# Kernel tuning notes

Hardware: AMD Instinct MI355X
Metric: run time of the kernel (lower is better)

The kernel has to match this reference:

```python
import jax, jax.numpy as jnp
import numpy as np

B, T, S = 16, 128, 128          # batch, temporal, spatial (road segments)
NIN, SIN = 3, 1                 # number / speed input feature sizes
NH, SH, DH = 64, 64, 128        # number-enc / speed-enc / decoder hidden
T_PREDICT = 20


def _p(k, shape, scale=0.05):
    return (jax.random.normal(k, shape) * scale).astype(jnp.float32)


def setup_inputs() -> dict:
    key = jax.random.key(0)
    ks = jax.random.split(key, 16)
    inp = {"input_data": jax.random.normal(ks[0], (B, T, S, NIN + SIN), dtype=jnp.float32)}
    # seg_model cells: LSTM gates driven by input x, own hidden h, spatial neighbors h_after/h_before
    inp.update(
        n_Wx=_p(ks[1], (NIN, 4 * NH)), n_Wh=_p(ks[2], (NH, 4 * NH)),
        n_Wa=_p(ks[3], (NH, 4 * NH)), n_Wb=_p(ks[4], (NH, 4 * NH)),
        n_b=jnp.zeros((4 * NH,), jnp.float32),
        s_Wx=_p(ks[5], (SIN, 4 * SH)), s_Wh=_p(ks[6], (SH, 4 * SH)),
        s_Wa=_p(ks[7], (SH, 4 * SH)), s_Wb=_p(ks[8], (SH, 4 * SH)),
        s_b=jnp.zeros((4 * SH,), jnp.float32),
        d_Wx=_p(ks[9], (NH + SH, 4 * DH)), d_Wh=_p(ks[10], (DH, 4 * DH)),
        d_Wa=_p(ks[11], (DH, 4 * DH)), d_Wb=_p(ks[12], (DH, 4 * DH)),
        d_b=jnp.zeros((4 * DH,), jnp.float32),
        on_W=_p(ks[13], (DH, 1)), on_b=jnp.zeros((1,), jnp.float32),
        os_W=_p(ks[14], (DH, 1)), os_b=jnp.zeros((1,), jnp.float32),
    )
    return inp


def _cell(x, h, c, ha, hb, Wx, Wh, Wa, Wb, b):
    g = x @ Wx + h @ Wh + ha @ Wa + hb @ Wb + b
    i, f, u, o = jnp.split(g, 4, axis=-1)
    c2 = jax.nn.sigmoid(f) * c + jax.nn.sigmoid(i) * jnp.tanh(u)
    return jax.nn.sigmoid(o) * jnp.tanh(c2), c2


def _shift(h):
    # h_after[s] = h[s+1], h_before[s] = h[s-1], zero-padded at the boundary
    z = jnp.zeros_like(h[:, :1])
    return jnp.concatenate([h[:, 1:], z], axis=1), jnp.concatenate([z, h[:, :-1]], axis=1)


def _next_input(former_number, next_x, output):
    # output: [B,S,2] = (number_out, speed_out)
    speed_in = next_x[:, :1, 3:]                                    # [B,1,1]
    speed_next = jnp.concatenate([speed_in, output[:, 1:, 1:]], axis=1)
    inflow = jnp.concatenate([next_x[:, 0:1, 1:2], output[:, :-1, 0:1]], axis=1)
    number_calc = former_number[:, :, 2:3] + inflow - output[:, :, 0:1]
    return jnp.concatenate([output[:, :, 0:1], inflow, number_calc, speed_next], axis=2)


def reference(input_data, n_Wx, n_Wh, n_Wa, n_Wb, n_b,
              s_Wx, s_Wh, s_Wa, s_Wb, s_b,
              d_Wx, d_Wh, d_Wa, d_Wb, d_b,
              on_W, on_b, os_W, os_b):
    b, t, s, _ = input_data.shape
    zeros = lambda hdim: jnp.zeros((b, s, hdim), input_data.dtype)
    init = (zeros(NH), zeros(NH), zeros(SH), zeros(SH), zeros(DH), zeros(DH))

    def step(carry, xs):
        hn, cn, hs, cs, hd, cd = carry
        x_t, x_tp1 = xs
        hn_a, hn_b = _shift(hn)
        hs_a, hs_b = _shift(hs)
        hd_a, hd_b = _shift(hd)
        num = x_t[:, :, :NIN]
        spd = x_t[:, :, NIN:]
        hn, cn = _cell(num, hn, cn, hn_a, hn_b, n_Wx, n_Wh, n_Wa, n_Wb, n_b)
        hs, cs = _cell(spd, hs, cs, hs_a, hs_b, s_Wx, s_Wh, s_Wa, s_Wb, s_b)
        dec_in = jnp.concatenate([hn, hs], axis=2)
        hd, cd = _cell(dec_in, hd, cd, hd_a, hd_b, d_Wx, d_Wh, d_Wa, d_Wb, d_b)
        output = jnp.concatenate([hd @ on_W + on_b, hd @ os_W + os_b], axis=2)
        data = _next_input(num, x_tp1, output)
        return (hn, cn, hs, cs, hd, cd), data

    xs = (jnp.moveaxis(input_data[:, :-1], 1, 0),   # x_t,   t = 0..T-2 (time-major)
          jnp.moveaxis(input_data[:, 1:], 1, 0))    # x_{t+1}
    _, datas = jax.lax.scan(step, init, xs)          # [T-1, B, S, 4]
    # original writes outputs only for time >= t_predict; slicing is equivalent
    return jnp.moveaxis(datas[T_PREDICT:], 0, 1)     # [B, T-T_PREDICT-1, S, 4]
```

## Files before the change

### kernel.cpp

```cpp
#include <hip/hip_runtime.h>

constexpr int B_ = 16, T_ = 128, S_ = 128;
constexpr int ROWS = B_ * S_;
constexpr int NSTEPS = T_ - 1;
constexpr int TPRED = 20;
constexpr int TOUT = NSTEPS - TPRED;
constexpr int TB = 512;
constexpr int NBLK = 160;

constexpr int OFF_HN = 0;
constexpr int OFF_HS = OFF_HN + 262144;
constexpr int OFF_HD = OFF_HS + 262144;
constexpr int OFF_BAR = OFF_HD + 262144;
constexpr int OFF_OUTS = OFF_BAR + 8192;
constexpr int OFF_NPK = OFF_OUTS + NSTEPS * ROWS * 2;
constexpr int NPK_DW = 16 * 7 * 256;
constexpr int OFF_SPK = OFF_NPK + NPK_DW;
constexpr int OFF_DPK = OFF_SPK + NPK_DW;
constexpr int DPK_DW = 32 * 16 * 256;
constexpr int PACK_DWORDS = 2 * NPK_DW + DPK_DW;
constexpr int ZERO_DW = OFF_NPK;

typedef _Float16 half8 __attribute__((ext_vector_type(8)));
typedef float float4v __attribute__((ext_vector_type(4)));
typedef unsigned long long ull;

__device__ __forceinline__ float sigm(float x) { return 1.f / (1.f + __expf(-x)); }
__device__ __forceinline__ float tanh_(float x) { return 2.f / (1.f + __expf(-2.f * x)) - 1.f; }
__device__ __forceinline__ unsigned int pack2(float a, float b) {
    union { unsigned int u; _Float16 h[2]; } x;
    x.h[0] = (_Float16)a; x.h[1] = (_Float16)b; return x.u;
}

__device__ __forceinline__ unsigned ld_dev_u32(const unsigned* p) {
    return __hip_atomic_load(p, __ATOMIC_RELAXED, __HIP_MEMORY_SCOPE_AGENT);
}
__device__ __forceinline__ ull ld_dev_u64(const ull* p) {
    return __hip_atomic_load(p, __ATOMIC_RELAXED, __HIP_MEMORY_SCOPE_AGENT);
}
__device__ __forceinline__ void st_dev_u64(ull* p, ull v) {
    __hip_atomic_store(p, v, __ATOMIC_RELAXED, __HIP_MEMORY_SCOPE_AGENT);
}
__device__ __forceinline__ void st_dev_f16(_Float16* p, _Float16 v) {
    __hip_atomic_store(p, v, __ATOMIC_RELAXED, __HIP_MEMORY_SCOPE_AGENT);
}
__device__ __forceinline__ void at_add_u32(unsigned* p, unsigned v) {
    __hip_atomic_fetch_add(p, v, __ATOMIC_RELAXED, __HIP_MEMORY_SCOPE_AGENT);
}
__device__ __forceinline__ void at_add_f32(float* p, float v) {
    __hip_atomic_fetch_add(p, v, __ATOMIC_RELAXED, __HIP_MEMORY_SCOPE_AGENT);
}

__global__ __launch_bounds__(256) void pack_weights(
    const float* __restrict__ nWx, const float* __restrict__ nWh,
    const float* __restrict__ nWa, const float* __restrict__ nWb, const float* __restrict__ nb,
    const float* __restrict__ sWx, const float* __restrict__ sWh,
    const float* __restrict__ sWa, const float* __restrict__ sWb, const float* __restrict__ sb,
    const float* __restrict__ dWx, const float* __restrict__ dWh,
    const float* __restrict__ dWa, const float* __restrict__ dWb,
    unsigned int* __restrict__ wsu)
{
    int idx = blockIdx.x * 256 + threadIdx.x;
    if (idx >= PACK_DWORDS) return;
    if (idx < 2 * NPK_DW) {
        bool isS = idx >= NPK_DW;
        int dn = isS ? idx - NPK_DW : idx;
        int tile = dn >> 8;
        int e = (dn & 255) * 2;
        int lane = e >> 3, j0 = e & 7;
        int quad = lane >> 4;
        int nt = tile / 7, tt = tile % 7;
        int col = nt * 16 + (lane & 15);
        float v0, v1;
        if (tt < 6) {
            const float* W = isS ? ((tt < 2) ? sWh : (tt < 4) ? sWa : sWb)
                                 : ((tt < 2) ? nWh : (tt < 4) ? nWa : nWb);
            int k = (tt & 1) * 32 + quad * 8 + j0;
            v0 = W[k * 256 + col]; v1 = W[(k + 1) * 256 + col];
        } else {
            int kl = quad * 8 + j0;
            auto xv = [&](int k) -> float {
                if (!isS) { if (k < 3) return nWx[k * 256 + col]; if (k == 3) return nb[col]; return 0.f; }
                else      { if (k == 4) return sWx[col]; if (k == 5) return sb[col]; return 0.f; }
            };
            v0 = xv(kl); v1 = xv(kl + 1);
        }
        wsu[(isS ? OFF_SPK : OFF_NPK) + dn] = pack2(v0, v1);
    } else {
        int dd = idx - 2 * NPK_DW;
        int tile = dd >> 8;
        int e = (dd & 255) * 2;
        int lane = e >> 3, j0 = e & 7;
        int quad = lane >> 4;
        int nt = tile >> 4, tt = tile & 15;
        const float* W = (tt < 4) ? dWx : (tt < 8) ? dWh : (tt < 12) ? dWa : dWb;
        int k = (tt & 3) * 32 + quad * 8 + j0;
        int col = nt * 16 + (lane & 15);
        wsu[OFF_DPK + dd] = pack2(W[k * 512 + col], W[(k + 1) * 512 + col]);
    }
}

__global__ __launch_bounds__(TB) void pipe_persist(
    const float* __restrict__ input,
    const float* __restrict__ db,
    const float* __restrict__ onW, const float* __restrict__ onb,
    const float* __restrict__ osW, const float* __restrict__ osb,
    float* __restrict__ ws)
{
    const int tid = threadIdx.x;
    const int wave = tid >> 6, lane = tid & 63;
    const int quad = lane >> 4, l15 = lane & 15;
    const int blk = blockIdx.x;

    unsigned* wsu = (unsigned*)ws;
    unsigned* hnU = wsu + OFF_HN;
    unsigned* hsU = wsu + OFF_HS;
    unsigned* hdU = wsu + OFF_HD;
    unsigned* nsc = wsu + OFF_BAR;
    unsigned* dc  = wsu + OFF_BAR + 1024;
    float* outs = ws + OFF_OUTS;

    union SMem {
        struct {
            _Float16 pk[16 * 7 * 512];
            _Float16 hst[2][130][72];
            _Float16 xa[128][40];
        } ns;
        struct {
            _Float16 wd[4 * 16 * 512];
            _Float16 dec[128][136];
            _Float16 hd[130][136];
            _Float16 hpub[128][16];
        } d;
    };
    __shared__ __align__(16) SMem sm;

    if (blk < 32) {
        const bool isS = (blk >= 16);
        const int rg = blk & 15;
        _Float16* hH = (_Float16*)(isS ? hsU : hnU);
        unsigned* dcp = dc + rg * 32;

        const ull* pkG = (const ull*)(wsu + (isS ? OFF_SPK : OFF_NPK));
        for (int i = tid; i < 14336; i += TB) ((ull*)sm.ns.pk)[i] = pkG[i];
        for (int i = tid; i < 9360; i += TB) ((unsigned*)sm.ns.hst)[i] = 0u;
        for (int i = tid; i < 2560; i += TB) ((unsigned*)sm.ns.xa)[i] = 0u;
        float4v c4[4];
#pragma unroll
        for (int cg = 0; cg < 4; ++cg) c4[cg] = (float4v){0.f, 0.f, 0.f, 0.f};
        __syncthreads();

        for (int e = 0; e < NSTEPS; ++e) {
            const int pinL = (e + 1) & 1, poutL = e & 1;
            const int poutG = e & 3;
            if (tid < 128) {
                const float* xp = input + ((size_t)(rg * T_ + e) * S_ + tid) * 4;
                unsigned* row = (unsigned*)sm.ns.xa + tid * 20;
                row[0] = pack2(xp[0], xp[1]);
                row[1] = pack2(xp[2], 1.f);
                row[2] = pack2(xp[3], 1.f);
            }
            if (e >= 4) {
                unsigned tgt = 8u * (unsigned)(e - 3);
                while (ld_dev_u32(dcp) < tgt) __builtin_amdgcn_s_sleep(1);
            }
            __syncthreads();

            const _Float16* hb = &sm.ns.hst[pinL][0][0];
            const int ri = wave * 16 + l15;
            half8 ah0 = *(const half8*)(hb + (ri + 1) * 72 + quad * 8);
            half8 ah1 = *(const half8*)(hb + (ri + 1) * 72 + 32 + quad * 8);
            half8 aa0 = *(const half8*)(hb + (ri + 2) * 72 + quad * 8);
            half8 aa1 = *(const half8*)(hb + (ri + 2) * 72 + 32 + quad * 8);
            half8 ab0 = *(const half8*)(hb + (ri) * 72 + quad * 8);
            half8 ab1 = *(const half8*)(hb + (ri) * 72 + 32 + quad * 8);
            half8 ax  = *(const half8*)(&sm.ns.xa[0][0] + ri * 40 + quad * 8);
            _Float16* hLp = &sm.ns.hst[poutL][0][0];
            _Float16* hGp = hH + (size_t)poutG * 131072 + (size_t)rg * 128 * 64;
#pragma unroll
            for (int cg = 0; cg < 4; ++cg) {
                float4v acc[4];
#pragma unroll
                for (int g = 0; g < 4; ++g) acc[g] = (float4v){0.f, 0.f, 0.f, 0.f};
#pragma unroll
                for (int g = 0; g < 4; ++g) {
                    const _Float16* base = sm.ns.pk + (size_t)(4 * g + cg) * 7 * 512 + lane * 8;
                    acc[g] = __builtin_amdgcn_mfma_f32_16x16x32_f16(ah0, *(const half8*)(base),        acc[g], 0, 0, 0);
                    acc[g] = __builtin_amdgcn_mfma_f32_16x16x32_f16(ah1, *(const half8*)(base + 512),  acc[g], 0, 0, 0);
                    acc[g] = __builtin_amdgcn_mfma_f32_16x16x32_f16(aa0, *(const half8*)(base + 1024), acc[g], 0, 0, 0);
                    acc[g] = __builtin_amdgcn_mfma_f32_16x16x32_f16(aa1, *(const half8*)(base + 1536), acc[g], 0, 0, 0);
                    acc[g] = __builtin_amdgcn_mfma_f32_16x16x32_f16(ab0, *(const half8*)(base + 2048), acc[g], 0, 0, 0);
                    acc[g] = __builtin_amdgcn_mfma_f32_16x16x32_f16(ab1, *(const half8*)(base + 2560), acc[g], 0, 0, 0);
                    acc[g] = __builtin_amdgcn_mfma_f32_16x16x32_f16(ax,  *(const half8*)(base + 3072), acc[g], 0, 0, 0);
                }
                const int kcol = cg * 16 + l15;
                float4v cold = c4[cg], cnew;
#pragma unroll
                for (int r = 0; r < 4; ++r) {
                    float c2 = sigm(acc[1][r]) * cold[r] + sigm(acc[0][r]) * tanh_(acc[2][r]);
                    float h2 = sigm(acc[3][r]) * tanh_(c2);
                    cnew[r] = c2;
                    int row = wave * 16 + quad * 4 + r;
                    _Float16 hf = (_Float16)h2;
                    hLp[(row + 1) * 72 + kcol] = hf;
                    st_dev_f16(hGp + (size_t)row * 64 + kcol, hf);
                }
                c4[cg] = cnew;
            }
            asm volatile("s_waitcnt vmcnt(0)" ::: "memory");
            __syncthreads();
            if (tid == 0) at_add_u32(nsc + rg * 32, 1u);
        }
    } else {
        const int idx = blk - 32;
        const int rg = idx >> 3;
        const int c = idx & 7;
        const int r0 = rg * 128;
        unsigned* dcp = dc + rg * 32;
        unsigned* nscp = nsc + rg * 32;

        const ull* pdG = (const ull*)(wsu + OFF_DPK);
        for (int i = tid; i < 8192; i += TB) {
            int tile = i >> 7, j = i & 127;
            int g = tile >> 4, tt = tile & 15;
            ((ull*)sm.d.wd)[(g * 16 + tt) * 128 + j] =
                pdG[(size_t)((g * 8 + c) * 16 + tt) * 128 + j];
        }
        if (tid < 68) {
            ((unsigned*)&sm.d.hd[0][0])[tid] = 0u;
            ((unsigned*)&sm.d.hd[129][0])[tid] = 0u;
        }
        const int hcol = c * 16 + l15;
        const float won = onW[hcol], wos = osW[hcol];
        float bg[4];
#pragma unroll
        for (int g = 0; g < 4; ++g) bg[g] = db[g * 128 + hcol];
        float4v creg = (float4v){0.f, 0.f, 0.f, 0.f};
        __syncthreads();

        for (int e = 1; e <= NSTEPS; ++e) {
            const int t = e - 1;
            const int pdec = t & 3;
            const int phdin = e & 1;
            const int phdout = t & 1;
            if (e >= 2) {
                unsigned tgt = 8u * (unsigned)(e - 1);
                while (ld_dev_u32(dcp) < tgt) __builtin_amdgcn_s_sleep(1);
            }
            {
                unsigned tgt = 2u * (unsigned)e;
                while (ld_dev_u32(nscp) < tgt) __builtin_amdgcn_s_sleep(1);
            }
            const ull* srcH = (const ull*)(hdU + (size_t)phdin * 131072);
#pragma unroll
            for (int i = tid; i < 4096; i += TB) {
                int row = i >> 5, j = i & 31;
                *((ull*)&sm.d.hd[row + 1][0] + j) = ld_dev_u64(srcH + (size_t)(r0 + row) * 32 + j);
            }
            const ull* srcN = (const ull*)(hnU + (size_t)pdec * 32768);
            const ull* srcS = (const ull*)(hsU + (size_t)pdec * 32768);
#pragma unroll
            for (int i = tid; i < 4096; i += TB) {
                int hf = i >> 11, j2 = i & 2047;
                int row = j2 >> 4, j = j2 & 15;
                *((ull*)&sm.d.dec[row][hf * 64] + j) =
                    ld_dev_u64((hf ? srcS : srcN) + (size_t)(r0 + row) * 16 + j);
            }
            __syncthreads();

            const int ri = wave * 16 + l15;
            half8 fr[16];
#pragma unroll
            for (int kt = 0; kt < 4; ++kt) {
                fr[kt]      = *(const half8*)(&sm.d.dec[ri][0] + kt * 32 + quad * 8);
                fr[4 + kt]  = *(const half8*)(&sm.d.hd[ri + 1][0] + kt * 32 + quad * 8);
                fr[8 + kt]  = *(const half8*)(&sm.d.hd[ri + 2][0] + kt * 32 + quad * 8);
                fr[12 + kt] = *(const half8*)(&sm.d.hd[ri][0] + kt * 32 + quad * 8);
            }
            float4v acc[4];
#pragma unroll
            for (int g = 0; g < 4; ++g) acc[g] = (float4v){0.f, 0.f, 0.f, 0.f};
#pragma unroll
            for (int g = 0; g < 4; ++g) {
                const _Float16* bw = sm.d.wd + (size_t)(g * 16) * 512 + lane * 8;
#pragma unroll
                for (int kt = 0; kt < 16; ++kt)
                    acc[g] = __builtin_amdgcn_mfma_f32_16x16x32_f16(fr[kt], *(const half8*)(bw + kt * 512), acc[g], 0, 0, 0);
            }
            float4v cold = creg, cnew;
#pragma unroll
            for (int r = 0; r < 4; ++r) {
                float c2 = sigm(acc[1][r] + bg[1]) * cold[r] + sigm(acc[0][r] + bg[0]) * tanh_(acc[2][r] + bg[2]);
                float h2 = sigm(acc[3][r] + bg[3]) * tanh_(c2);
                cnew[r] = c2;
                int row = wave * 16 + quad * 4 + r;
                sm.d.hpub[row][l15] = (_Float16)h2;
                float pon = h2 * won, pos = h2 * wos;
#pragma unroll
                for (int off = 8; off; off >>= 1) {
                    pon += __shfl_down(pon, off, 16);
                    pos += __shfl_down(pos, off, 16);
                }
                if (l15 == 0) {
                    float* o = outs + ((size_t)t * ROWS + (r0 + row)) * 2;
                    at_add_f32(o, pon);
                    at_add_f32(o + 1, pos);
                }
            }
            creg = cnew;
            __syncthreads();
            {
                int prow = tid >> 2, jj = tid & 3;
                ull v = *((const ull*)&sm.d.hpub[prow][0] + jj);
                st_dev_u64((ull*)hdU + (size_t)phdout * 65536 + (size_t)(r0 + prow) * 32 + c * 4 + jj, v);
            }
            asm volatile("s_waitcnt vmcnt(0)" ::: "memory");
            __syncthreads();
            if (tid == 0) at_add_u32(dcp, 1u);
        }
    }
}

__global__ __launch_bounds__(256) void assemble_kernel(
    const float* __restrict__ input, const float* __restrict__ ws, float* __restrict__ out,
    const float* __restrict__ onb, const float* __restrict__ osb)
{
    const float* outs = ws + OFF_OUTS;
    int idx = blockIdx.x * 256 + threadIdx.x;
    if (idx >= B_ * TOUT * S_) return;
    float b_on = onb[0], b_os = osb[0];
    int s = idx & 127;
    int tmp = idx >> 7;
    int tt = tmp % TOUT;
    int b = tmp / TOUT;
    int t = tt + TPRED;
    int row = b * S_ + s;
    float o0 = outs[((size_t)t * ROWS + row) * 2 + 0] + b_on;
    float o1 = outs[((size_t)t * ROWS + row) * 2 + 1] + b_os;
    float inflow = (s == 0) ? input[(((size_t)b * T_ + (t + 1)) * S_ + 0) * 4 + 1]
                            : (outs[((size_t)t * ROWS + row - 1) * 2 + 0] + b_on);
    float numc = input[(((size_t)b * T_ + t) * S_ + s) * 4 + 2] + inflow - o0;
    float spd = (s == 0) ? input[(((size_t)b * T_ + (t + 1)) * S_ + 0) * 4 + 3] : o1;
    float4 v = make_float4(o0, inflow, numc, spd);
    reinterpret_cast<float4*>(out)[idx] = v;
}

extern "C" void kernel_launch(void* const* d_in, const int* in_sizes, int n_in,
                              void* d_out, int out_size, void* d_ws, size_t ws_size,
                              hipStream_t stream) {
    const float* input = (const float*)d_in[0];
    const float* nWx = (const float*)d_in[1];
    const float* nWh = (const float*)d_in[2];
    const float* nWa = (const float*)d_in[3];
    const float* nWb = (const float*)d_in[4];
    const float* nb  = (const float*)d_in[5];
    const float* sWx = (const float*)d_in[6];
    const float* sWh = (const float*)d_in[7];
    const float* sWa = (const float*)d_in[8];
    const float* sWb = (const float*)d_in[9];
    const float* sb  = (const float*)d_in[10];
    const float* dWx = (const float*)d_in[11];
    const float* dWh = (const float*)d_in[12];
    const float* dWa = (const float*)d_in[13];
    const float* dWb = (const float*)d_in[14];
    const float* db  = (const float*)d_in[15];
    const float* onW = (const float*)d_in[16];
    const float* onb = (const float*)d_in[17];
    const float* osW = (const float*)d_in[18];
    const float* osb = (const float*)d_in[19];

    float* ws = (float*)d_ws;

    hipMemsetAsync(ws, 0, (size_t)ZERO_DW * 4, stream);

    pack_weights<<<dim3((PACK_DWORDS + 255) / 256), dim3(256), 0, stream>>>(
        nWx, nWh, nWa, nWb, nb, sWx, sWh, sWa, sWb, sb,
        dWx, dWh, dWa, dWb, (unsigned int*)ws);

    void* kargs[] = {
        (void*)&input, (void*)&db, (void*)&onW, (void*)&onb,
        (void*)&osW, (void*)&osb, (void*)&ws
    };
    hipLaunchCooperativeKernel((void*)pipe_persist, dim3(NBLK), dim3(TB),
                               kargs, 0, stream);

    int nout = B_ * TOUT * S_;
    assemble_kernel<<<dim3((nout + 255) / 256), dim3(256), 0, stream>>>(
        input, ws, (float*)d_out, onb, osb);
}
```

Baseline: 1.317 ms.

## Batch hidden-state publishes and reorder decoder waits to overlap loads with signaling

Encoder blocks now write their hidden state to shared memory only, then publish it to global memory with coalesced 64-bit stores after a barrier, replacing scattered per-element f16 atomic stores. Decoder blocks wait on the encoder counter first and load the encoder outputs before waiting on the decoder-neighbor counter, with loads batched into registers. The decoder also signals its step completion before the output-projection atomics, which shortens the critical path between dependent blocks. This adds an extra barrier in the encoder and keeps more registers live for the staged loads.

```diff
diff --git a/kernel.cpp b/kernel.cpp
--- a/kernel.cpp
+++ b/kernel.cpp
@@ -41,15 +41,13 @@
 __device__ __forceinline__ void st_dev_u64(ull* p, ull v) {
     __hip_atomic_store(p, v, __ATOMIC_RELAXED, __HIP_MEMORY_SCOPE_AGENT);
 }
-__device__ __forceinline__ void st_dev_f16(_Float16* p, _Float16 v) {
-    __hip_atomic_store(p, v, __ATOMIC_RELAXED, __HIP_MEMORY_SCOPE_AGENT);
-}
 __device__ __forceinline__ void at_add_u32(unsigned* p, unsigned v) {
     __hip_atomic_fetch_add(p, v, __ATOMIC_RELAXED, __HIP_MEMORY_SCOPE_AGENT);
 }
 __device__ __forceinline__ void at_add_f32(float* p, float v) {
     __hip_atomic_fetch_add(p, v, __ATOMIC_RELAXED, __HIP_MEMORY_SCOPE_AGENT);
 }
+#define WAIT_VM0() asm volatile("s_waitcnt vmcnt(0)" ::: "memory")
 
 __global__ __launch_bounds__(256) void pack_weights(
     const float* __restrict__ nWx, const float* __restrict__ nWh,
@@ -113,9 +111,9 @@
     const int blk = blockIdx.x;
 
     unsigned* wsu = (unsigned*)ws;
-    unsigned* hnU = wsu + OFF_HN;
-    unsigned* hsU = wsu + OFF_HS;
-    unsigned* hdU = wsu + OFF_HD;
+    char* hnB = (char*)(wsu + OFF_HN);
+    char* hsB = (char*)(wsu + OFF_HS);
+    char* hdB = (char*)(wsu + OFF_HD);
     unsigned* nsc = wsu + OFF_BAR;
     unsigned* dc  = wsu + OFF_BAR + 1024;
     float* outs = ws + OFF_OUTS;
@@ -138,8 +136,9 @@
     if (blk < 32) {
         const bool isS = (blk >= 16);
         const int rg = blk & 15;
-        _Float16* hH = (_Float16*)(isS ? hsU : hnU);
+        char* hB = isS ? hsB : hnB;
         unsigned* dcp = dc + rg * 32;
+        unsigned* nscp = nsc + rg * 32;
 
         const ull* pkG = (const ull*)(wsu + (isS ? OFF_SPK : OFF_NPK));
         for (int i = tid; i < 14336; i += TB) ((ull*)sm.ns.pk)[i] = pkG[i];
@@ -176,7 +175,6 @@
             half8 ab1 = *(const half8*)(hb + (ri) * 72 + 32 + quad * 8);
             half8 ax  = *(const half8*)(&sm.ns.xa[0][0] + ri * 40 + quad * 8);
             _Float16* hLp = &sm.ns.hst[poutL][0][0];
-            _Float16* hGp = hH + (size_t)poutG * 131072 + (size_t)rg * 128 * 64;
 #pragma unroll
             for (int cg = 0; cg < 4; ++cg) {
                 float4v acc[4];
@@ -201,15 +199,24 @@
                     float h2 = sigm(acc[3][r]) * tanh_(c2);
                     cnew[r] = c2;
                     int row = wave * 16 + quad * 4 + r;
-                    _Float16 hf = (_Float16)h2;
-                    hLp[(row + 1) * 72 + kcol] = hf;
-                    st_dev_f16(hGp + (size_t)row * 64 + kcol, hf);
+                    hLp[(row + 1) * 72 + kcol] = (_Float16)h2;
                 }
                 c4[cg] = cnew;
             }
-            asm volatile("s_waitcnt vmcnt(0)" ::: "memory");
-            __syncthreads();
-            if (tid == 0) at_add_u32(nsc + rg * 32, 1u);
+            __syncthreads();
+            {
+                char* dst0 = hB + (size_t)poutG * 262144 + (size_t)rg * 16384;
+#pragma unroll
+                for (int k = 0; k < 4; ++k) {
+                    int i = tid + k * 512;
+                    int row = i >> 4, j = i & 15;
+                    ull v = *((const ull*)&sm.ns.hst[poutL][row + 1][0] + j);
+                    st_dev_u64((ull*)(dst0 + (size_t)row * 128 + (size_t)j * 8), v);
+                }
+            }
+            WAIT_VM0();
+            __syncthreads();
+            if (tid == 0) at_add_u32(nscp, 1u);
         }
     } else {
         const int idx = blk - 32;
@@ -243,28 +250,46 @@
             const int pdec = t & 3;
             const int phdin = e & 1;
             const int phdout = t & 1;
+            {
+                unsigned tgt = 2u * (unsigned)e;
+                while (ld_dev_u32(nscp) < tgt) __builtin_amdgcn_s_sleep(1);
+            }
+            {
+                ull t8[8];
+#pragma unroll
+                for (int k = 0; k < 8; ++k) {
+                    int i = tid + k * 512;
+                    int row = i >> 5, j = i & 31;
+                    const char* src = (j < 16 ? hnB : hsB) + (size_t)pdec * 262144
+                                      + (size_t)(r0 + row) * 128 + (size_t)(j & 15) * 8;
+                    t8[k] = ld_dev_u64((const ull*)src);
+                }
+#pragma unroll
+                for (int k = 0; k < 8; ++k) {
+                    int i = tid + k * 512;
+                    int row = i >> 5, j = i & 31;
+                    *((ull*)&sm.d.dec[row][0] + j) = t8[k];
+                }
+            }
             if (e >= 2) {
                 unsigned tgt = 8u * (unsigned)(e - 1);
                 while (ld_dev_u32(dcp) < tgt) __builtin_amdgcn_s_sleep(1);
             }
             {
-                unsigned tgt = 2u * (unsigned)e;
-                while (ld_dev_u32(nscp) < tgt) __builtin_amdgcn_s_sleep(1);
-            }
-            const ull* srcH = (const ull*)(hdU + (size_t)phdin * 131072);
-#pragma unroll
-            for (int i = tid; i < 4096; i += TB) {
-                int row = i >> 5, j = i & 31;
-                *((ull*)&sm.d.hd[row + 1][0] + j) = ld_dev_u64(srcH + (size_t)(r0 + row) * 32 + j);
-            }
-            const ull* srcN = (const ull*)(hnU + (size_t)pdec * 32768);
-            const ull* srcS = (const ull*)(hsU + (size_t)pdec * 32768);
-#pragma unroll
-            for (int i = tid; i < 4096; i += TB) {
-                int hf = i >> 11, j2 = i & 2047;
-                int row = j2 >> 4, j = j2 & 15;
-                *((ull*)&sm.d.dec[row][hf * 64] + j) =
-                    ld_dev_u64((hf ? srcS : srcN) + (size_t)(r0 + row) * 16 + j);
+                ull t8[8];
+#pragma unroll
+                for (int k = 0; k < 8; ++k) {
+                    int i = tid + k * 512;
+                    int row = i >> 5, j = i & 31;
+                    t8[k] = ld_dev_u64((const ull*)(hdB + (size_t)phdin * 524288
+                                       + (size_t)(r0 + row) * 256 + (size_t)j * 8));
+                }
+#pragma unroll
+                for (int k = 0; k < 8; ++k) {
+                    int i = tid + k * 512;
+                    int row = i >> 5, j = i & 31;
+                    *((ull*)&sm.d.hd[row + 1][0] + j) = t8[k];
+                }
             }
             __syncthreads();
 
@@ -288,14 +313,31 @@
                     acc[g] = __builtin_amdgcn_mfma_f32_16x16x32_f16(fr[kt], *(const half8*)(bw + kt * 512), acc[g], 0, 0, 0);
             }
             float4v cold = creg, cnew;
+            float h2s[4];
 #pragma unroll
             for (int r = 0; r < 4; ++r) {
                 float c2 = sigm(acc[1][r] + bg[1]) * cold[r] + sigm(acc[0][r] + bg[0]) * tanh_(acc[2][r] + bg[2]);
                 float h2 = sigm(acc[3][r] + bg[3]) * tanh_(c2);
                 cnew[r] = c2;
+                h2s[r] = h2;
                 int row = wave * 16 + quad * 4 + r;
                 sm.d.hpub[row][l15] = (_Float16)h2;
-                float pon = h2 * won, pos = h2 * wos;
+            }
+            creg = cnew;
+            __syncthreads();
+            {
+                int prow = tid >> 2, jj = tid & 3;
+                ull v = *((const ull*)&sm.d.hpub[prow][0] + jj);
+                st_dev_u64((ull*)(hdB + (size_t)phdout * 524288 + (size_t)(r0 + prow) * 256
+                           + (size_t)c * 32 + (size_t)jj * 8), v);
+            }
+            WAIT_VM0();
+            __syncthreads();
+            if (tid == 0) at_add_u32(dcp, 1u);
+#pragma unroll
+            for (int r = 0; r < 4; ++r) {
+                int row = wave * 16 + quad * 4 + r;
+                float pon = h2s[r] * won, pos = h2s[r] * wos;
 #pragma unroll
                 for (int off = 8; off; off >>= 1) {
                     pon += __shfl_down(pon, off, 16);
@@ -307,16 +349,6 @@
                     at_add_f32(o + 1, pos);
                 }
             }
-            creg = cnew;
-            __syncthreads();
-            {
-                int prow = tid >> 2, jj = tid & 3;
-                ull v = *((const ull*)&sm.d.hpub[prow][0] + jj);
-                st_dev_u64((ull*)hdU + (size_t)phdout * 65536 + (size_t)(r0 + prow) * 32 + c * 4 + jj, v);
-            }
-            asm volatile("s_waitcnt vmcnt(0)" ::: "memory");
-            __syncthreads();
-            if (tid == 0) at_add_u32(dcp, 1u);
         }
     }
 }
```

Result: faster. 1.186 ms (-10.0%).
